# Kernel tuning notes

Measured on AMD Instinct MI355X. Metric: run time of the kernel, lower is better.

The kernel has to match this reference:

```python
import jax, jax.numpy as jnp
import numpy as np

B, S, C = 2, 2048, 512
E, H = 512, 8
HD = E // H
SCALE = HD ** -0.5


def setup_inputs() -> dict:
    key = jax.random.key(0)
    ks = jax.random.split(key, 10)
    s = 1.0 / np.sqrt(C)
    return {
        "x": jax.random.normal(ks[0], (B, S, C), dtype=jnp.float32),
        "dist_map": jax.random.uniform(ks[1], (B, H, S, S), dtype=jnp.float32),
        "mask": jax.random.randint(ks[2], (B, S), 0, 2, dtype=jnp.int32),
        "Wq": jax.random.normal(ks[3], (E, C), dtype=jnp.float32) * s,
        "bq": jnp.zeros((E,), dtype=jnp.float32),
        "Wk": jax.random.normal(ks[4], (E, C), dtype=jnp.float32) * s,
        "bk": jnp.zeros((E,), dtype=jnp.float32),
        "Wv": jax.random.normal(ks[5], (E, C), dtype=jnp.float32) * s,
        "bv": jnp.zeros((E,), dtype=jnp.float32),
        "Wo": jax.random.normal(ks[6], (E, E), dtype=jnp.float32) * (1.0 / np.sqrt(E)),
        "bo": jnp.zeros((E,), dtype=jnp.float32),
    }


def reference(x, dist_map, mask, Wq, bq, Wk, bk, Wv, bv, Wo, bo):
    # NOTE: faithful to original torch code: .view(B, H, S, HD) without transpose
    q = (x @ Wq.T + bq).reshape(B, H, S, HD)
    k = (x @ Wk.T + bk).reshape(B, H, S, HD)
    v = (x @ Wv.T + bv).reshape(B, H, S, HD)
    attn = jnp.einsum('bhqd,bhkd->bhqk', q, k)
    pad = mask.astype(bool)[:, None, None, :]  # [B,1,1,S]
    attn = jnp.where(pad, jnp.float32(-10000.0), attn)
    attn = jax.nn.softmax(attn * SCALE, axis=-1)
    attn = (attn + dist_map) * 0.5  # post-softmax dist_map blend
    # dropout p=0.0 -> identity
    attn_probs = attn
    ctx = jnp.einsum('bhal,bhlv->bhav', attn_probs, v)  # [B,H,S,HD]
    ctx = ctx.transpose(0, 2, 1, 3).reshape(B, S, E)
    out = ctx @ Wo.T + bo
    return (out, attn_probs)
```

## Files before the change

kernel.cpp:

```cpp
#include <hip/hip_runtime.h>
#include <stdint.h>

typedef __attribute__((ext_vector_type(4))) float  f32x4;
typedef __attribute__((ext_vector_type(8))) short  short8;
typedef __attribute__((ext_vector_type(4))) short  short4v;

#define MFMA16(a,b,c) __builtin_amdgcn_mfma_f32_16x16x32_bf16((a),(b),(c),0,0,0)

typedef __attribute__((address_space(1))) void gv_t;
typedef __attribute__((address_space(3))) void lv_t;
#define GLL16(g,l) __builtin_amdgcn_global_load_lds((const gv_t*)(g), (lv_t*)(l), 16, 0, 0)

static __device__ __forceinline__ unsigned short f2bf(float f) {
    unsigned int u = __float_as_uint(f);
    u += 0x7FFFu + ((u >> 16) & 1u);
    return (unsigned short)(u >> 16);
}
static __device__ __forceinline__ float bflo(unsigned int v) { return __uint_as_float(v << 16); }
static __device__ __forceinline__ float bfhi(unsigned int v) { return __uint_as_float(v & 0xFFFF0000u); }
static __device__ __forceinline__ float bf2f(unsigned short v) { return __uint_as_float(((unsigned int)v) << 16); }
static __device__ __forceinline__ unsigned int packbf(float a, float b) {
    return (unsigned int)f2bf(a) | ((unsigned int)f2bf(b) << 16);
}


__global__ __launch_bounds__(256) void qkv_gemm(
    const float* __restrict__ x,
    const float* __restrict__ Wq, const float* __restrict__ bq,
    const float* __restrict__ Wk, const float* __restrict__ bk,
    const float* __restrict__ Wv, const float* __restrict__ bv,
    unsigned short* __restrict__ Qb, unsigned short* __restrict__ Kb,
    unsigned short* __restrict__ Vb)
{
    __shared__ unsigned short As[128 * 40];
    __shared__ unsigned short Bs[128 * 40];

    const int tid  = threadIdx.x;
    const int lane = tid & 63;
    const int wid  = tid >> 6;
    const int g = lane >> 4, c = lane & 15;
    const int wr = wid >> 1, wc = wid & 1;
    const int bm    = blockIdx.x;
    const int widx  = blockIdx.y >> 2;
    const int ntile = blockIdx.y & 3;

    const float* W    = (widx == 0) ? Wq : (widx == 1) ? Wk : Wv;
    const float* bias = (widx == 0) ? bq : (widx == 1) ? bk : bv;
    unsigned short* Y = (widx == 0) ? Qb : (widx == 1) ? Kb : Vb;
    const float* Abase = x + (size_t)bm * 128 * 512;
    const float* Bbase = W + (size_t)ntile * 128 * 512;

    f32x4 acc[4][4];
    #pragma unroll
    for (int m = 0; m < 4; m++)
        #pragma unroll
        for (int n = 0; n < 4; n++) acc[m][n] = (f32x4){0.f, 0.f, 0.f, 0.f};

    for (int kk = 0; kk < 512; kk += 32) {
        #pragma unroll
        for (int i = 0; i < 4; i++) {
            int f  = i * 256 + tid;
            int rr = f >> 3;
            int cc = (f & 7) * 4;
            f32x4 va = *(const f32x4*)(Abase + rr * 512 + kk + cc);
            f32x4 vb = *(const f32x4*)(Bbase + rr * 512 + kk + cc);
            short4v sa, sb;
            #pragma unroll
            for (int q = 0; q < 4; q++) { sa[q] = (short)f2bf(va[q]); sb[q] = (short)f2bf(vb[q]); }
            *(short4v*)(&As[rr * 40 + cc]) = sa;
            *(short4v*)(&Bs[rr * 40 + cc]) = sb;
        }
        __syncthreads();

        short8 af[4], bfr[4];
        #pragma unroll
        for (int m = 0; m < 4; m++) af[m]  = *(const short8*)(&As[(wr * 64 + m * 16 + c) * 40 + g * 8]);
        #pragma unroll
        for (int n = 0; n < 4; n++) bfr[n] = *(const short8*)(&Bs[(wc * 64 + n * 16 + c) * 40 + g * 8]);
        #pragma unroll
        for (int m = 0; m < 4; m++)
            #pragma unroll
            for (int n = 0; n < 4; n++)
                acc[m][n] = MFMA16(af[m], bfr[n], acc[m][n]);
        __syncthreads();
    }

    #pragma unroll
    for (int n = 0; n < 4; n++) {
        int colW = ntile * 128 + wc * 64 + n * 16 + c;
        float bb = bias[colW];
        #pragma unroll
        for (int m = 0; m < 4; m++) {
            #pragma unroll
            for (int r = 0; r < 4; r++) {
                int row = bm * 128 + wr * 64 + m * 16 + g * 4 + r;
                Y[(size_t)row * 512 + colW] = f2bf(acc[m][n][r] + bb);
            }
        }
    }
}

__global__ __launch_bounds__(256) void v_transpose(
    const unsigned short* __restrict__ Vb, unsigned short* __restrict__ Vt)
{
    __shared__ unsigned short T[8][520];

    const int tid = threadIdx.x;
    const int t   = blockIdx.x;
    const int bh  = blockIdx.y;
    const int b = bh >> 3, h = bh & 7;

    #pragma unroll
    for (int i = 0; i < 2; i++) {
        int idx = i * 256 + tid;
        int j   = idx >> 6;
        int cc  = (idx & 63) * 8;
        short8 v = *(const short8*)(Vb + (size_t)(b * 2048 + h * 256 + t * 8 + j) * 512 + cc);
        *(short8*)(&T[j][cc]) = v;
    }
    __syncthreads();

    const int d   = tid >> 2;
    const int sjb = (tid & 3) * 16;
    unsigned short tmp[16];
    #pragma unroll
    for (int i = 0; i < 16; i++) {
        int sj = sjb + i;
        tmp[i] = T[sj >> 3][(sj & 7) * 64 + d];
    }
    unsigned short* dst = Vt + ((size_t)(bh * 64 + d) * 2048) + t * 64 + sjb;
    *(short8*)(dst)     = *(short8*)(&tmp[0]);
    *(short8*)(dst + 8) = *(short8*)(&tmp[8]);
}

__global__ __launch_bounds__(256) void attn_kernel(
    const unsigned short* __restrict__ Qb, const unsigned short* __restrict__ Kb,
    const unsigned short* __restrict__ Vt,
    const float* __restrict__ dist, const int* __restrict__ mask,
    float* __restrict__ attn_out, unsigned short* __restrict__ ctx_bf)
{
    __shared__ unsigned short AP[4][16][72];
    __shared__ float red[4][2][16];
    __shared__ __attribute__((aligned(16))) float UN[8192];

    const int tid = threadIdx.x;
    const int lane = tid & 63, wid = tid >> 6;
    const int g = lane >> 4, c = lane & 15;

    const int wg  = blockIdx.x + gridDim.x * blockIdx.y;
    const int qg  = (wg >> 3) & 127;
    const int bh  = (wg & 7) * 2 + ((wg >> 10) & 1);
    const int b = bh >> 3, h = bh & 7;

    const unsigned short* Qh  = Qb + (size_t)b * 1048576 + (size_t)h * 131072;
    const unsigned short* Kh  = Kb + (size_t)b * 1048576 + (size_t)h * 131072;
    const unsigned short* Vth = Vt + (size_t)bh * 131072;
    const float* distb = dist + (size_t)bh * 4194304;
    float*       outb  = attn_out + (size_t)bh * 4194304;
    const int*   maskb = mask + b * 2048;

    const int qrow    = qg * 16;
    const int keybase = wid * 512;

    const float SC      = 0.18033688011f;
    const float MASKVAL = -1803.3688f;

    short8 qf[2];
    #pragma unroll
    for (int ks = 0; ks < 2; ks++)
        qf[ks] = *(const short8*)(Qh + (size_t)(qrow + c) * 64 + ks * 32 + g * 8);

    unsigned int pl[8][4][2];
    float lmax[4] = {-3e38f, -3e38f, -3e38f, -3e38f};

    #pragma unroll
    for (int kb8 = 0; kb8 < 8; kb8++) {
        const int kb = keybase + kb8 * 64;
        short8 kf[4][2];
        #pragma unroll
        for (int n = 0; n < 4; n++)
            #pragma unroll
            for (int ks = 0; ks < 2; ks++)
                kf[n][ks] = *(const short8*)(Kh + (size_t)(kb + n * 16 + c) * 64 + ks * 32 + g * 8);
        #pragma unroll
        for (int n = 0; n < 4; n++) {
            f32x4 z = (f32x4){0.f, 0.f, 0.f, 0.f};
            z = MFMA16(qf[0], kf[n][0], z);
            z = MFMA16(qf[1], kf[n][1], z);
            const int mv = maskb[kb + n * 16 + c];
            float l[4];
            #pragma unroll
            for (int r = 0; r < 4; r++) {
                l[r] = mv ? MASKVAL : z[r] * SC;
                lmax[r] = fmaxf(lmax[r], l[r]);
            }
            pl[kb8][n][0] = packbf(l[0], l[1]);
            pl[kb8][n][1] = packbf(l[2], l[3]);
        }
    }
    #pragma unroll
    for (int r = 0; r < 4; r++) {
        #pragma unroll
        for (int off = 1; off < 16; off <<= 1)
            lmax[r] = fmaxf(lmax[r], __shfl_xor(lmax[r], off));
    }
    if (c == 0) {
        #pragma unroll
        for (int r = 0; r < 4; r++) red[wid][0][g * 4 + r] = lmax[r];
    }
    __syncthreads();
    float m[4];
    #pragma unroll
    for (int r = 0; r < 4; r++) {
        int row = g * 4 + r;
        m[r] = fmaxf(fmaxf(red[0][0][row], red[1][0][row]),
                     fmaxf(red[2][0][row], red[3][0][row]));
    }

    float dsum[4] = {0.f, 0.f, 0.f, 0.f};
    #pragma unroll
    for (int kb8 = 0; kb8 < 8; kb8++) {
        #pragma unroll
        for (int n = 0; n < 4; n++) {
            #pragma unroll
            for (int pi = 0; pi < 2; pi++) {
                unsigned int v = pl[kb8][n][pi];
                float e0 = exp2f(bflo(v) - m[pi * 2]);
                float e1 = exp2f(bfhi(v) - m[pi * 2 + 1]);
                dsum[pi * 2]     += e0;
                dsum[pi * 2 + 1] += e1;
                pl[kb8][n][pi] = packbf(e0, e1);
            }
        }
    }
    #pragma unroll
    for (int r = 0; r < 4; r++) {
        #pragma unroll
        for (int off = 1; off < 16; off <<= 1)
            dsum[r] += __shfl_xor(dsum[r], off);
    }
    if (c == 0) {
        #pragma unroll
        for (int r = 0; r < 4; r++) red[wid][1][g * 4 + r] = dsum[r];
    }
    __syncthreads();
    float invd[4];
    #pragma unroll
    for (int r = 0; r < 4; r++) {
        int row = g * 4 + r;
        invd[r] = 1.f / (red[0][1][row] + red[1][1][row] + red[2][1][row] + red[3][1][row]);
    }

    f32x4 cacc[4];
    #pragma unroll
    for (int nd = 0; nd < 4; nd++) cacc[nd] = (f32x4){0.f, 0.f, 0.f, 0.f};

    const float* dsrc = distb + (size_t)(qrow + (lane >> 4)) * 2048 + keybase + (lane & 15) * 4;
    float* stg0 = &UN[wid * 2048];
    float* stg1 = stg0 + 1024;

    #pragma unroll
    for (int ch = 0; ch < 4; ch++)
        GLL16(dsrc + ch * 4 * 2048, stg0 + ch * 256);
    __syncthreads();

    #pragma unroll
    for (int t = 0; t < 8; t++) {
        const int kb = keybase + t * 64;
        float* cur = (t & 1) ? stg1 : stg0;
        float* nxt = (t & 1) ? stg0 : stg1;

        if (t < 7) {
            const float* ns = dsrc + (t + 1) * 64;
            #pragma unroll
            for (int ch = 0; ch < 4; ch++)
                GLL16(ns + ch * 4 * 2048, nxt + ch * 256);
        }

        #pragma unroll
        for (int n = 0; n < 4; n++) {
            #pragma unroll
            for (int pi = 0; pi < 2; pi++) {
                unsigned int v = pl[t][n][pi];
                AP[wid][g * 4 + pi * 2    ][n * 16 + c] = f2bf(bflo(v) * invd[pi * 2]);
                AP[wid][g * 4 + pi * 2 + 1][n * 16 + c] = f2bf(bfhi(v) * invd[pi * 2 + 1]);
            }
        }

        #pragma unroll
        for (int rg = 0; rg < 4; rg++) {
            const int row = rg * 4 + g;
            f32x4 dvv = *(const f32x4*)(cur + row * 64 + c * 4);
            short4v pv = *(const short4v*)(&AP[wid][row][c * 4]);
            f32x4 apv;
            #pragma unroll
            for (int q = 0; q < 4; q++)
                apv[q] = 0.5f * (bf2f((unsigned short)pv[q]) + dvv[q]);
            *(f32x4*)(outb + (size_t)(qrow + row) * 2048 + kb + c * 4) = apv;
            short4v apb;
            #pragma unroll
            for (int q = 0; q < 4; q++) apb[q] = (short)f2bf(apv[q]);
            *(short4v*)(&AP[wid][row][c * 4]) = apb;
        }

        short8 apf[2];
        #pragma unroll
        for (int ks = 0; ks < 2; ks++)
            apf[ks] = *(const short8*)(&AP[wid][c][ks * 32 + g * 8]);
        #pragma unroll
        for (int nd = 0; nd < 4; nd++) {
            #pragma unroll
            for (int ks = 0; ks < 2; ks++) {
                short8 vf = *(const short8*)(Vth + (size_t)(nd * 16 + c) * 2048 + kb + ks * 32 + g * 8);
                cacc[nd] = MFMA16(apf[ks], vf, cacc[nd]);
            }
        }

        __syncthreads();
    }

    float (*Cred)[16][68] = (float (*)[16][68])UN;
    #pragma unroll
    for (int nd = 0; nd < 4; nd++)
        #pragma unroll
        for (int r = 0; r < 4; r++)
            Cred[wid][g * 4 + r][nd * 16 + c] = cacc[nd][r];
    __syncthreads();

    {
        const int q  = tid >> 4;
        const int dq = (tid & 15) * 4;
        f32x4 s = *(const f32x4*)(&Cred[0][q][dq]);
        #pragma unroll
        for (int w = 1; w < 4; w++) {
            f32x4 t2 = *(const f32x4*)(&Cred[w][q][dq]);
            #pragma unroll
            for (int j = 0; j < 4; j++) s[j] += t2[j];
        }
        short4v cb;
        #pragma unroll
        for (int j = 0; j < 4; j++) cb[j] = (short)f2bf(s[j]);
        *(short4v*)(ctx_bf + (size_t)(b * 2048 + qrow + q) * 512 + h * 64 + dq) = cb;
    }
}

__global__ __launch_bounds__(256) void out_gemm(
    const unsigned short* __restrict__ A,
    const float* __restrict__ Wo, const float* __restrict__ bo,
    float* __restrict__ out)
{
    __shared__ unsigned short As[128 * 40];
    __shared__ unsigned short Bs[128 * 40];

    const int tid  = threadIdx.x;
    const int lane = tid & 63;
    const int wid  = tid >> 6;
    const int g = lane >> 4, c = lane & 15;
    const int wr = wid >> 1, wc = wid & 1;
    const int bm    = blockIdx.x;
    const int ntile = blockIdx.y;

    const unsigned short* Abase = A + (size_t)bm * 128 * 512;
    const float* Bbase = Wo + (size_t)ntile * 128 * 512;

    f32x4 acc[4][4];
    #pragma unroll
    for (int m = 0; m < 4; m++)
        #pragma unroll
        for (int n = 0; n < 4; n++) acc[m][n] = (f32x4){0.f, 0.f, 0.f, 0.f};

    for (int kk = 0; kk < 512; kk += 32) {
        #pragma unroll
        for (int i = 0; i < 2; i++) {
            int f8 = i * 256 + tid;
            int rr = f8 >> 2;
            int cc = (f8 & 3) * 8;
            short8 va = *(const short8*)(Abase + (size_t)rr * 512 + kk + cc);
            *(short8*)(&As[rr * 40 + cc]) = va;
        }
        #pragma unroll
        for (int i = 0; i < 4; i++) {
            int f  = i * 256 + tid;
            int rr = f >> 3;
            int cc = (f & 7) * 4;
            f32x4 vb = *(const f32x4*)(Bbase + (size_t)rr * 512 + kk + cc);
            short4v sb;
            #pragma unroll
            for (int q = 0; q < 4; q++) sb[q] = (short)f2bf(vb[q]);
            *(short4v*)(&Bs[rr * 40 + cc]) = sb;
        }
        __syncthreads();

        short8 af[4], bfr[4];
        #pragma unroll
        for (int m = 0; m < 4; m++) af[m]  = *(const short8*)(&As[(wr * 64 + m * 16 + c) * 40 + g * 8]);
        #pragma unroll
        for (int n = 0; n < 4; n++) bfr[n] = *(const short8*)(&Bs[(wc * 64 + n * 16 + c) * 40 + g * 8]);
        #pragma unroll
        for (int m = 0; m < 4; m++)
            #pragma unroll
            for (int n = 0; n < 4; n++)
                acc[m][n] = MFMA16(af[m], bfr[n], acc[m][n]);
        __syncthreads();
    }

    #pragma unroll
    for (int n = 0; n < 4; n++) {
        int col = ntile * 128 + wc * 64 + n * 16 + c;
        float bb = bo[col];
        #pragma unroll
        for (int m = 0; m < 4; m++) {
            #pragma unroll
            for (int r = 0; r < 4; r++) {
                int row = bm * 128 + wr * 64 + m * 16 + g * 4 + r;
                out[(size_t)row * 512 + col] = acc[m][n][r] + bb;
            }
        }
    }
}

extern "C" void kernel_launch(void* const* d_in, const int* in_sizes, int n_in,
                              void* d_out, int out_size, void* d_ws, size_t ws_size,
                              hipStream_t stream)
{
    const float* x    = (const float*)d_in[0];
    const float* dist = (const float*)d_in[1];
    const int*   mask = (const int*)d_in[2];
    const float* Wq   = (const float*)d_in[3];
    const float* bq   = (const float*)d_in[4];
    const float* Wk   = (const float*)d_in[5];
    const float* bk   = (const float*)d_in[6];
    const float* Wv   = (const float*)d_in[7];
    const float* bv   = (const float*)d_in[8];
    const float* Wo   = (const float*)d_in[9];
    const float* bo   = (const float*)d_in[10];

    float* out      = (float*)d_out;
    float* attn_out = out + 2097152;

    char* ws = (char*)d_ws;
    unsigned short* Qb  = (unsigned short*)(ws);
    unsigned short* Kb  = (unsigned short*)(ws + (4u << 20));
    unsigned short* Vb  = (unsigned short*)(ws + (8u << 20));
    unsigned short* Vt  = (unsigned short*)(ws + (12u << 20));
    unsigned short* ctx = (unsigned short*)(ws + (8u << 20));

    qkv_gemm   <<<dim3(32, 12), 256, 0, stream>>>(x, Wq, bq, Wk, bk, Wv, bv, Qb, Kb, Vb);
    v_transpose<<<dim3(32, 16), 256, 0, stream>>>(Vb, Vt);
    attn_kernel<<<dim3(128, 16), 256, 0, stream>>>(Qb, Kb, Vt, dist, mask, attn_out, ctx);
    out_gemm   <<<dim3(32, 4),  256, 0, stream>>>(ctx, Wo, bo, out);
}
```

Before: 262.9 us.

## Recompute QK logits with online softmax stats instead of caching them in registers

Replaces the register-cached bf16 logits array (64 packed values per lane) with a two-pass scheme. The first pass computes running max and denominator online, and the second pass recomputes QK^T via MFMA and applies exp directly. Dist-map prefetch moves from global_load_lds LDS staging to register double-buffering, shared memory is shrunk and aliased, per-iteration barriers are removed, and attn stores become nontemporal. The aim is to cut register and LDS pressure and raise occupancy (launch bounds 256,4), at the cost of doubling QK MFMA work and K loads.

```diff
diff --git a/kernel.cpp b/kernel.cpp
--- a/kernel.cpp
+++ b/kernel.cpp
@@ -6,22 +6,13 @@
 typedef __attribute__((ext_vector_type(4))) short  short4v;
 
 #define MFMA16(a,b,c) __builtin_amdgcn_mfma_f32_16x16x32_bf16((a),(b),(c),0,0,0)
-
-typedef __attribute__((address_space(1))) void gv_t;
-typedef __attribute__((address_space(3))) void lv_t;
-#define GLL16(g,l) __builtin_amdgcn_global_load_lds((const gv_t*)(g), (lv_t*)(l), 16, 0, 0)
 
 static __device__ __forceinline__ unsigned short f2bf(float f) {
     unsigned int u = __float_as_uint(f);
     u += 0x7FFFu + ((u >> 16) & 1u);
     return (unsigned short)(u >> 16);
 }
-static __device__ __forceinline__ float bflo(unsigned int v) { return __uint_as_float(v << 16); }
-static __device__ __forceinline__ float bfhi(unsigned int v) { return __uint_as_float(v & 0xFFFF0000u); }
 static __device__ __forceinline__ float bf2f(unsigned short v) { return __uint_as_float(((unsigned int)v) << 16); }
-static __device__ __forceinline__ unsigned int packbf(float a, float b) {
-    return (unsigned int)f2bf(a) | ((unsigned int)f2bf(b) << 16);
-}
 
 
 __global__ __launch_bounds__(256) void qkv_gemm(
@@ -133,15 +124,16 @@
     *(short8*)(dst + 8) = *(short8*)(&tmp[8]);
 }
 
-__global__ __launch_bounds__(256) void attn_kernel(
+__global__ __launch_bounds__(256, 4) void attn_kernel(
     const unsigned short* __restrict__ Qb, const unsigned short* __restrict__ Kb,
     const unsigned short* __restrict__ Vt,
     const float* __restrict__ dist, const int* __restrict__ mask,
     float* __restrict__ attn_out, unsigned short* __restrict__ ctx_bf)
 {
-    __shared__ unsigned short AP[4][16][72];
     __shared__ float red[4][2][16];
-    __shared__ __attribute__((aligned(16))) float UN[8192];
+    __shared__ __attribute__((aligned(16))) unsigned char SMEM[17408];
+    unsigned short (*AP)[16][72] = (unsigned short (*)[16][72])SMEM;
+    float (*Cred)[16][68] = (float (*)[16][68])SMEM;
 
     const int tid = threadIdx.x;
     const int lane = tid & 63, wid = tid >> 6;
@@ -170,133 +162,113 @@
     for (int ks = 0; ks < 2; ks++)
         qf[ks] = *(const short8*)(Qh + (size_t)(qrow + c) * 64 + ks * 32 + g * 8);
 
-    unsigned int pl[8][4][2];
-    float lmax[4] = {-3e38f, -3e38f, -3e38f, -3e38f};
-
-    #pragma unroll
-    for (int kb8 = 0; kb8 < 8; kb8++) {
-        const int kb = keybase + kb8 * 64;
-        short8 kf[4][2];
-        #pragma unroll
-        for (int n = 0; n < 4; n++)
-            #pragma unroll
-            for (int ks = 0; ks < 2; ks++)
-                kf[n][ks] = *(const short8*)(Kh + (size_t)(kb + n * 16 + c) * 64 + ks * 32 + g * 8);
-        #pragma unroll
-        for (int n = 0; n < 4; n++) {
-            f32x4 z = (f32x4){0.f, 0.f, 0.f, 0.f};
-            z = MFMA16(qf[0], kf[n][0], z);
-            z = MFMA16(qf[1], kf[n][1], z);
-            const int mv = maskb[kb + n * 16 + c];
-            float l[4];
-            #pragma unroll
-            for (int r = 0; r < 4; r++) {
-                l[r] = mv ? MASKVAL : z[r] * SC;
-                lmax[r] = fmaxf(lmax[r], l[r]);
-            }
-            pl[kb8][n][0] = packbf(l[0], l[1]);
-            pl[kb8][n][1] = packbf(l[2], l[3]);
-        }
-    }
-    #pragma unroll
-    for (int r = 0; r < 4; r++) {
-        #pragma unroll
-        for (int off = 1; off < 16; off <<= 1)
-            lmax[r] = fmaxf(lmax[r], __shfl_xor(lmax[r], off));
-    }
-    if (c == 0) {
-        #pragma unroll
-        for (int r = 0; r < 4; r++) red[wid][0][g * 4 + r] = lmax[r];
-    }
-    __syncthreads();
-    float m[4];
-    #pragma unroll
-    for (int r = 0; r < 4; r++) {
-        int row = g * 4 + r;
-        m[r] = fmaxf(fmaxf(red[0][0][row], red[1][0][row]),
-                     fmaxf(red[2][0][row], red[3][0][row]));
-    }
-
-    float dsum[4] = {0.f, 0.f, 0.f, 0.f};
-    #pragma unroll
-    for (int kb8 = 0; kb8 < 8; kb8++) {
-        #pragma unroll
-        for (int n = 0; n < 4; n++) {
-            #pragma unroll
-            for (int pi = 0; pi < 2; pi++) {
-                unsigned int v = pl[kb8][n][pi];
-                float e0 = exp2f(bflo(v) - m[pi * 2]);
-                float e1 = exp2f(bfhi(v) - m[pi * 2 + 1]);
-                dsum[pi * 2]     += e0;
-                dsum[pi * 2 + 1] += e1;
-                pl[kb8][n][pi] = packbf(e0, e1);
-            }
-        }
-    }
-    #pragma unroll
-    for (int r = 0; r < 4; r++) {
-        #pragma unroll
-        for (int off = 1; off < 16; off <<= 1)
-            dsum[r] += __shfl_xor(dsum[r], off);
-    }
-    if (c == 0) {
-        #pragma unroll
-        for (int r = 0; r < 4; r++) red[wid][1][g * 4 + r] = dsum[r];
-    }
-    __syncthreads();
-    float invd[4];
-    #pragma unroll
-    for (int r = 0; r < 4; r++) {
-        int row = g * 4 + r;
-        invd[r] = 1.f / (red[0][1][row] + red[1][1][row] + red[2][1][row] + red[3][1][row]);
-    }
-
-    f32x4 cacc[4];
-    #pragma unroll
-    for (int nd = 0; nd < 4; nd++) cacc[nd] = (f32x4){0.f, 0.f, 0.f, 0.f};
-
-    const float* dsrc = distb + (size_t)(qrow + (lane >> 4)) * 2048 + keybase + (lane & 15) * 4;
-    float* stg0 = &UN[wid * 2048];
-    float* stg1 = stg0 + 1024;
-
-    #pragma unroll
-    for (int ch = 0; ch < 4; ch++)
-        GLL16(dsrc + ch * 4 * 2048, stg0 + ch * 256);
-    __syncthreads();
+    float mrun[4] = {-3e38f, -3e38f, -3e38f, -3e38f};
+    float drun[4] = {0.f, 0.f, 0.f, 0.f};
 
     #pragma unroll
     for (int t = 0; t < 8; t++) {
         const int kb = keybase + t * 64;
-        float* cur = (t & 1) ? stg1 : stg0;
-        float* nxt = (t & 1) ? stg0 : stg1;
-
+        float l[4][4];
+        #pragma unroll
+        for (int n = 0; n < 4; n++) {
+            short8 k0 = *(const short8*)(Kh + (size_t)(kb + n * 16 + c) * 64 + g * 8);
+            short8 k1 = *(const short8*)(Kh + (size_t)(kb + n * 16 + c) * 64 + 32 + g * 8);
+            f32x4 z = (f32x4){0.f, 0.f, 0.f, 0.f};
+            z = MFMA16(qf[0], k0, z);
+            z = MFMA16(qf[1], k1, z);
+            const int mv = maskb[kb + n * 16 + c];
+            #pragma unroll
+            for (int r = 0; r < 4; r++)
+                l[n][r] = mv ? MASKVAL : z[r] * SC;
+        }
+        #pragma unroll
+        for (int r = 0; r < 4; r++) {
+            float tm = fmaxf(fmaxf(l[0][r], l[1][r]), fmaxf(l[2][r], l[3][r]));
+            float mn = fmaxf(mrun[r], tm);
+            float s  = exp2f(l[0][r] - mn) + exp2f(l[1][r] - mn)
+                     + exp2f(l[2][r] - mn) + exp2f(l[3][r] - mn);
+            drun[r] = fmaf(drun[r], exp2f(mrun[r] - mn), s);
+            mrun[r] = mn;
+        }
+    }
+    #pragma unroll
+    for (int r = 0; r < 4; r++) {
+        #pragma unroll
+        for (int off = 1; off < 16; off <<= 1) {
+            float om = __shfl_xor(mrun[r], off);
+            float od = __shfl_xor(drun[r], off);
+            float mn = fmaxf(mrun[r], om);
+            drun[r] = drun[r] * exp2f(mrun[r] - mn) + od * exp2f(om - mn);
+            mrun[r] = mn;
+        }
+    }
+    if (c == 0) {
+        #pragma unroll
+        for (int r = 0; r < 4; r++) {
+            red[wid][0][g * 4 + r] = mrun[r];
+            red[wid][1][g * 4 + r] = drun[r];
+        }
+    }
+    __syncthreads();
+    float M[4], invd[4];
+    #pragma unroll
+    for (int r = 0; r < 4; r++) {
+        const int row = g * 4 + r;
+        float m0 = red[0][0][row], m1 = red[1][0][row];
+        float m2 = red[2][0][row], m3 = red[3][0][row];
+        float mm = fmaxf(fmaxf(m0, m1), fmaxf(m2, m3));
+        float D = red[0][1][row] * exp2f(m0 - mm) + red[1][1][row] * exp2f(m1 - mm)
+                + red[2][1][row] * exp2f(m2 - mm) + red[3][1][row] * exp2f(m3 - mm);
+        M[r] = mm;
+        invd[r] = 1.f / D;
+    }
+
+    f32x4 cacc[4];
+    #pragma unroll
+    for (int nd = 0; nd < 4; nd++) cacc[nd] = (f32x4){0.f, 0.f, 0.f, 0.f};
+
+    f32x4 dcur[4];
+    #pragma unroll
+    for (int rg = 0; rg < 4; rg++)
+        dcur[rg] = *(const f32x4*)(distb + (size_t)(qrow + rg * 4 + g) * 2048 + keybase + c * 4);
+
+    #pragma unroll
+    for (int t = 0; t < 8; t++) {
+        const int kb = keybase + t * 64;
+
+        f32x4 dnxt[4];
         if (t < 7) {
-            const float* ns = dsrc + (t + 1) * 64;
-            #pragma unroll
-            for (int ch = 0; ch < 4; ch++)
-                GLL16(ns + ch * 4 * 2048, nxt + ch * 256);
+            #pragma unroll
+            for (int rg = 0; rg < 4; rg++)
+                dnxt[rg] = *(const f32x4*)(distb + (size_t)(qrow + rg * 4 + g) * 2048 + kb + 64 + c * 4);
         }
 
         #pragma unroll
         for (int n = 0; n < 4; n++) {
-            #pragma unroll
-            for (int pi = 0; pi < 2; pi++) {
-                unsigned int v = pl[t][n][pi];
-                AP[wid][g * 4 + pi * 2    ][n * 16 + c] = f2bf(bflo(v) * invd[pi * 2]);
-                AP[wid][g * 4 + pi * 2 + 1][n * 16 + c] = f2bf(bfhi(v) * invd[pi * 2 + 1]);
+            short8 k0 = *(const short8*)(Kh + (size_t)(kb + n * 16 + c) * 64 + g * 8);
+            short8 k1 = *(const short8*)(Kh + (size_t)(kb + n * 16 + c) * 64 + 32 + g * 8);
+            f32x4 z = (f32x4){0.f, 0.f, 0.f, 0.f};
+            z = MFMA16(qf[0], k0, z);
+            z = MFMA16(qf[1], k1, z);
+            const int mv = maskb[kb + n * 16 + c];
+            #pragma unroll
+            for (int r = 0; r < 4; r++) {
+                float arg = fmaf(z[r], SC, -M[r]);
+                arg = mv ? -3000.f : arg;
+                float p = exp2f(arg) * invd[r];
+                AP[wid][g * 4 + r][n * 16 + c] = f2bf(p);
             }
         }
 
         #pragma unroll
         for (int rg = 0; rg < 4; rg++) {
             const int row = rg * 4 + g;
-            f32x4 dvv = *(const f32x4*)(cur + row * 64 + c * 4);
             short4v pv = *(const short4v*)(&AP[wid][row][c * 4]);
             f32x4 apv;
             #pragma unroll
             for (int q = 0; q < 4; q++)
-                apv[q] = 0.5f * (bf2f((unsigned short)pv[q]) + dvv[q]);
-            *(f32x4*)(outb + (size_t)(qrow + row) * 2048 + kb + c * 4) = apv;
+                apv[q] = 0.5f * (bf2f((unsigned short)pv[q]) + dcur[rg][q]);
+            __builtin_nontemporal_store(apv, (f32x4*)(outb + (size_t)(qrow + row) * 2048 + kb + c * 4));
             short4v apb;
             #pragma unroll
             for (int q = 0; q < 4; q++) apb[q] = (short)f2bf(apv[q]);
@@ -316,10 +288,11 @@
             }
         }
 
-        __syncthreads();
-    }
-
-    float (*Cred)[16][68] = (float (*)[16][68])UN;
+        #pragma unroll
+        for (int rg = 0; rg < 4; rg++) dcur[rg] = dnxt[rg];
+    }
+
+    __syncthreads();
     #pragma unroll
     for (int nd = 0; nd < 4; nd++)
         #pragma unroll
```

Measured after the change: 309.8 us. 1.18x slower.
